# Kernel optimization log

Measured on AMD Instinct MI355X. Metric: run time of the kernel, lower is better.

The kernel has to match this reference:

```python
import jax, jax.numpy as jnp
import numpy as np

N_NODES = 50000
N_EDGES = 600000
N_GRAPHS = 2000
IN_FEATS = 64
HIDDEN = 128


def setup_inputs() -> dict:
    key = jax.random.key(0)
    ks = jax.random.split(key, 16)
    d = {}
    d["feats_node"] = jax.random.normal(ks[0], (N_NODES, IN_FEATS), jnp.float32)
    d["feats_graph"] = jax.random.normal(ks[1], (N_GRAPHS, 3), jnp.float32)
    s = 0.05
    d["W1"] = jax.random.normal(ks[2], (IN_FEATS, HIDDEN), jnp.float32) * s
    d["b1"] = jnp.zeros((HIDDEN,), jnp.float32)
    d["W2"] = jax.random.normal(ks[3], (HIDDEN, HIDDEN), jnp.float32) * s
    d["b2"] = jnp.zeros((HIDDEN,), jnp.float32)
    d["W3"] = jax.random.normal(ks[4], (HIDDEN, HIDDEN), jnp.float32) * s
    d["b3"] = jnp.zeros((HIDDEN,), jnp.float32)
    d["Wl1"] = jax.random.normal(ks[5], (HIDDEN + 3, 2 * HIDDEN), jnp.float32) * s
    d["bl1"] = jnp.zeros((2 * HIDDEN,), jnp.float32)
    d["Wl2"] = jax.random.normal(ks[6], (2 * HIDDEN, 2 * HIDDEN), jnp.float32) * s
    d["bl2"] = jnp.zeros((2 * HIDDEN,), jnp.float32)
    d["Wl3"] = jax.random.normal(ks[7], (2 * HIDDEN, 1), jnp.float32) * s
    d["bl3"] = jnp.zeros((1,), jnp.float32)
    d["src"] = jax.random.randint(ks[8], (N_EDGES,), 0, N_NODES, jnp.int32)
    d["dst"] = jax.random.randint(ks[9], (N_EDGES,), 0, N_NODES, jnp.int32)
    d["graph_ids"] = jnp.sort(jax.random.randint(ks[10], (N_NODES,), 0, N_GRAPHS, jnp.int32))
    return d


def reference(feats_node, feats_graph, W1, b1, W2, b2, W3, b3,
              Wl1, bl1, Wl2, bl2, Wl3, bl3, src, dst, graph_ids):
    N = feats_node.shape[0]
    ones_e = jnp.ones((src.shape[0],), feats_node.dtype)
    # DGL GraphConv norm='both': symmetric degree normalization, degrees clamped to >=1
    deg_out = jax.ops.segment_sum(ones_e, src, num_segments=N)
    deg_in = jax.ops.segment_sum(ones_e, dst, num_segments=N)
    c_out = jax.lax.rsqrt(jnp.maximum(deg_out, 1.0))[:, None]  # [N,1]
    c_in = jax.lax.rsqrt(jnp.maximum(deg_in, 1.0))[:, None]

    def gconv(x, W, b):
        h = x * c_out                                   # scale by src out-degree
        agg = jax.ops.segment_sum(h[src], dst, num_segments=N)  # gather + scatter-add
        return (agg * c_in) @ W + b

    x = jax.nn.relu(gconv(feats_node, W1, b1))
    x = jax.nn.relu(gconv(x, W2, b2))
    y_nodes = gconv(x, W3, b3)                          # [N, HIDDEN]

    # readout_nodes op='mean' over batched graphs
    G = feats_graph.shape[0]
    sum_y = jax.ops.segment_sum(y_nodes, graph_ids, num_segments=G)
    cnt = jax.ops.segment_sum(jnp.ones((N,), y_nodes.dtype), graph_ids, num_segments=G)
    mean_y = sum_y / jnp.maximum(cnt, 1.0)[:, None]     # [G, HIDDEN]

    y = jnp.concatenate([mean_y, feats_graph], axis=1)  # [G, HIDDEN+3]
    y = jax.nn.relu(y @ Wl1 + bl1)
    y = jax.nn.relu(y @ Wl2 + bl2)
    return (y @ Wl3 + bl3).reshape(-1)                  # [G]
```

## Files before the change

### kernel.cpp

```cpp
#include <hip/hip_runtime.h>

constexpr int NNODES = 50000;
constexpr int NEDGES = 600000;
constexpr int NGRAPH = 2000;
constexpr int F0     = 64;
constexpr int H      = 128;
constexpr int H2     = 256;
constexpr int NB     = 49;

static __device__ __forceinline__ void fma4(float4& acc, float s, const float4& w) {
    acc.x = fmaf(s, w.x, acc.x);
    acc.y = fmaf(s, w.y, acc.y);
    acc.z = fmaf(s, w.z, acc.z);
    acc.w = fmaf(s, w.w, acc.w);
}

__global__ void k_deg(const int* __restrict__ src, const int* __restrict__ dst,
                      int* __restrict__ dout, int* __restrict__ din) {
    int t = blockIdx.x * 256 + threadIdx.x;
    if (t * 4 >= NEDGES) return;
    int4 s4 = ((const int4*)src)[t];
    int4 d4 = ((const int4*)dst)[t];
    atomicAdd(&dout[s4.x], 1);
    atomicAdd(&dout[s4.y], 1);
    atomicAdd(&dout[s4.z], 1);
    atomicAdd(&dout[s4.w], 1);
    atomicAdd(&din[d4.x], 1);
    atomicAdd(&din[d4.y], 1);
    atomicAdd(&din[d4.z], 1);
    atomicAdd(&din[d4.w], 1);
}

__global__ __launch_bounds__(1024) void k_scan1(const int* __restrict__ deg,
                                                int* __restrict__ row_start,
                                                int* __restrict__ partials,
                                                float* __restrict__ c_in) {
    __shared__ int wsum[16];
    int idx  = blockIdx.x * 1024 + threadIdx.x;
    int lane = threadIdx.x & 63;
    int wid  = threadIdx.x >> 6;
    int v = (idx < NNODES) ? deg[idx] : 0;
    if (idx < NNODES) c_in[idx] = rsqrtf(fmaxf((float)v, 1.0f));
    int incl = v;
#pragma unroll
    for (int off = 1; off < 64; off <<= 1) {
        int t = __shfl_up(incl, off);
        if (lane >= off) incl += t;
    }
    if (lane == 63) wsum[wid] = incl;
    __syncthreads();
    if (wid == 0) {
        int w = (lane < 16) ? wsum[lane] : 0;
        int wincl = w;
#pragma unroll
        for (int off = 1; off < 16; off <<= 1) {
            int t = __shfl_up(wincl, off);
            if (lane >= off) wincl += t;
        }
        if (lane < 16) wsum[lane] = wincl - w;
    }
    __syncthreads();
    int excl = wsum[wid] + incl - v;
    if (idx < NNODES) row_start[idx] = excl;
    if (threadIdx.x == 1023) partials[blockIdx.x] = excl + v;
}

__global__ void k_scan2(int* __restrict__ partials) {
    int lane = threadIdx.x;
    int v = (lane < NB) ? partials[lane] : 0;
    int incl = v;
#pragma unroll
    for (int off = 1; off < 64; off <<= 1) {
        int t = __shfl_up(incl, off);
        if (lane >= off) incl += t;
    }
    if (lane < NB) partials[lane] = incl - v;
    if (lane == NB - 1) partials[NB] = incl;
}

__global__ __launch_bounds__(1024) void k_scan3(int* __restrict__ row_start,
                                                const int* __restrict__ partials,
                                                const int* __restrict__ dout,
                                                float* __restrict__ c_out) {
    int idx = blockIdx.x * 1024 + threadIdx.x;
    if (idx < NNODES) {
        row_start[idx] += partials[blockIdx.x];
        c_out[idx] = rsqrtf(fmaxf((float)dout[idx], 1.0f));
    } else if (idx == NNODES) {
        row_start[NNODES] = partials[NB];
    }
}

__global__ void k_fill(const int* __restrict__ src, const int* __restrict__ dst,
                       const int* __restrict__ row_start, int* __restrict__ cursor,
                       int* __restrict__ csr_src) {
    int t = blockIdx.x * 256 + threadIdx.x;
    if (t * 4 >= NEDGES) return;
    int4 s4 = ((const int4*)src)[t];
    int4 d4 = ((const int4*)dst)[t];
    int p;
    p = atomicAdd(&cursor[d4.x], 1); csr_src[row_start[d4.x] + p] = s4.x;
    p = atomicAdd(&cursor[d4.y], 1); csr_src[row_start[d4.y] + p] = s4.y;
    p = atomicAdd(&cursor[d4.z], 1); csr_src[row_start[d4.z] + p] = s4.z;
    p = atomicAdd(&cursor[d4.w], 1); csr_src[row_start[d4.w] + p] = s4.w;
}

__global__ void k_gbounds(const int* __restrict__ gids, int* __restrict__ gstart) {
    int n = blockIdx.x * 256 + threadIdx.x;
    if (n > NNODES) return;
    if (n == 0) {
        int g0 = gids[0];
        for (int g = 0; g <= g0; ++g) gstart[g] = 0;
    } else if (n == NNODES) {
        int gl = gids[NNODES - 1];
        for (int g = gl + 1; g <= NGRAPH; ++g) gstart[g] = NNODES;
    } else {
        int a = gids[n - 1], b = gids[n];
        for (int g = a + 1; g <= b; ++g) gstart[g] = n;
    }
}

template <int F>
__global__ __launch_bounds__(256) void k_gather(const float* __restrict__ x,
                                                const float* __restrict__ c_out,
                                                const int* __restrict__ row_start,
                                                const int* __restrict__ csr_src,
                                                float* __restrict__ agg) {
    int wid  = (blockIdx.x * 256 + threadIdx.x) >> 6;
    int lane = threadIdx.x & 63;
    int h = lane >> 5, q = lane & 31;
    if (wid >= NNODES) return;
    int beg = row_start[wid], end = row_start[wid + 1];
    if (F == 128) {
        const float4* x4 = (const float4*)x;
        float4 acc = make_float4(0.f, 0.f, 0.f, 0.f);
        for (int i = beg + h; i < end; i += 2) {
            int s = csr_src[i];
            float co = c_out[s];
            float4 v = x4[(long)s * 32 + q];
            acc.x += v.x * co;
            acc.y += v.y * co;
            acc.z += v.z * co;
            acc.w += v.w * co;
        }
        acc.x += __shfl_xor(acc.x, 32);
        acc.y += __shfl_xor(acc.y, 32);
        acc.z += __shfl_xor(acc.z, 32);
        acc.w += __shfl_xor(acc.w, 32);
        if (h == 0) ((float4*)agg)[(long)wid * 32 + q] = acc;
    } else {
        const float2* x2 = (const float2*)x;
        float2 acc = make_float2(0.f, 0.f);
        for (int i = beg + h; i < end; i += 2) {
            int s = csr_src[i];
            float co = c_out[s];
            float2 v = x2[(long)s * 32 + q];
            acc.x += v.x * co;
            acc.y += v.y * co;
        }
        acc.x += __shfl_xor(acc.x, 32);
        acc.y += __shfl_xor(acc.y, 32);
        if (h == 0) ((float2*)agg)[(long)wid * 32 + q] = acc;
    }
}

template <int K, bool RELU>
__global__ __launch_bounds__(512) void k_gemm(const float* __restrict__ A,
                                              const float* __restrict__ c_in,
                                              const float* __restrict__ W,
                                              const float* __restrict__ b,
                                              float* __restrict__ out) {
    __shared__ float sW[K * H];
    for (int i = threadIdx.x; i < K * (H / 4); i += 512)
        ((float4*)sW)[i] = ((const float4*)W)[i];
    __syncthreads();

    const int c = threadIdx.x & 31;
    const int r = threadIdx.x >> 5;
    const long base = (long)blockIdx.x * 128 + r * 8;

    float4 acc[8];
#pragma unroll
    for (int i = 0; i < 8; ++i) acc[i] = make_float4(0.f, 0.f, 0.f, 0.f);

    const float4* Ap = (const float4*)A + base * (K / 4);

    for (int k4 = 0; k4 < K / 4; ++k4) {
        const float4 w0 = *(const float4*)&sW[(4 * k4 + 0) * H + 4 * c];
        const float4 w1 = *(const float4*)&sW[(4 * k4 + 1) * H + 4 * c];
        const float4 w2 = *(const float4*)&sW[(4 * k4 + 2) * H + 4 * c];
        const float4 w3 = *(const float4*)&sW[(4 * k4 + 3) * H + 4 * c];
#pragma unroll
        for (int i = 0; i < 8; ++i) {
            float4 a = Ap[(long)i * (K / 4) + k4];
            fma4(acc[i], a.x, w0);
            fma4(acc[i], a.y, w1);
            fma4(acc[i], a.z, w2);
            fma4(acc[i], a.w, w3);
        }
    }

    const float4 bv = ((const float4*)b)[c];
#pragma unroll
    for (int i = 0; i < 8; ++i) {
        long n = base + i;
        if (n < NNODES) {
            float ci = c_in[n];
            float4 res;
            res.x = fmaf(acc[i].x, ci, bv.x);
            res.y = fmaf(acc[i].y, ci, bv.y);
            res.z = fmaf(acc[i].z, ci, bv.z);
            res.w = fmaf(acc[i].w, ci, bv.w);
            if (RELU) {
                res.x = fmaxf(res.x, 0.f);
                res.y = fmaxf(res.y, 0.f);
                res.z = fmaxf(res.z, 0.f);
                res.w = fmaxf(res.w, 0.f);
            }
            ((float4*)out)[n * (H / 4) + c] = res;
        }
    }
}

__global__ void k_readout(const float* __restrict__ y, const int* __restrict__ gstart,
                          float* __restrict__ mean) {
    int g = blockIdx.x * 2 + (threadIdx.x >> 7);
    int j = threadIdx.x & 127;
    if (g >= NGRAPH) return;
    int beg = gstart[g], end = gstart[g + 1];
    float acc = 0.f;
    for (int n = beg; n < end; ++n) acc += y[(long)n * H + j];
    mean[g * H + j] = acc / fmaxf((float)(end - beg), 1.0f);
}

__global__ void k_mlp1(const float* __restrict__ mean, const float* __restrict__ fg,
                       const float* __restrict__ Wl1, const float* __restrict__ bl1,
                       float* __restrict__ h1) {
    int g  = blockIdx.x * 4 + (threadIdx.x >> 6);
    int jq = threadIdx.x & 63;
    if (g >= NGRAPH) return;
    float4 acc = ((const float4*)bl1)[jq];
    for (int k = 0; k < H; ++k)
        fma4(acc, mean[g * H + k], ((const float4*)(Wl1 + (long)k * H2))[jq]);
    for (int k = 0; k < 3; ++k)
        fma4(acc, fg[g * 3 + k], ((const float4*)(Wl1 + (long)(H + k) * H2))[jq]);
    acc.x = fmaxf(acc.x, 0.f); acc.y = fmaxf(acc.y, 0.f);
    acc.z = fmaxf(acc.z, 0.f); acc.w = fmaxf(acc.w, 0.f);
    ((float4*)h1)[g * 64 + jq] = acc;
}

__global__ void k_mlp2(const float* __restrict__ h1, const float* __restrict__ Wl2,
                       const float* __restrict__ bl2, float* __restrict__ h2) {
    int g  = blockIdx.x * 4 + (threadIdx.x >> 6);
    int jq = threadIdx.x & 63;
    if (g >= NGRAPH) return;
    float4 acc = ((const float4*)bl2)[jq];
    for (int k = 0; k < H2; ++k)
        fma4(acc, h1[g * H2 + k], ((const float4*)(Wl2 + (long)k * H2))[jq]);
    acc.x = fmaxf(acc.x, 0.f); acc.y = fmaxf(acc.y, 0.f);
    acc.z = fmaxf(acc.z, 0.f); acc.w = fmaxf(acc.w, 0.f);
    ((float4*)h2)[g * 64 + jq] = acc;
}

__global__ void k_mlp3(const float* __restrict__ h2, const float* __restrict__ Wl3,
                       const float* __restrict__ bl3, float* __restrict__ out) {
    int gw = (blockIdx.x * 256 + threadIdx.x) >> 6;
    int lane = threadIdx.x & 63;
    if (gw >= NGRAPH) return;
    float sum = 0.0f;
    for (int k = lane; k < H2; k += 64)
        sum += h2[gw * H2 + k] * Wl3[k];
    for (int off = 32; off; off >>= 1)
        sum += __shfl_down(sum, off);
    if (lane == 0) out[gw] = sum + bl3[0];
}

extern "C" void kernel_launch(void* const* d_in, const int* in_sizes, int n_in,
                              void* d_out, int out_size, void* d_ws, size_t ws_size,
                              hipStream_t stream) {
    const float* feats_node  = (const float*)d_in[0];
    const float* feats_graph = (const float*)d_in[1];
    const float* W1 = (const float*)d_in[2];
    const float* b1 = (const float*)d_in[3];
    const float* W2 = (const float*)d_in[4];
    const float* b2 = (const float*)d_in[5];
    const float* W3 = (const float*)d_in[6];
    const float* b3 = (const float*)d_in[7];
    const float* Wl1 = (const float*)d_in[8];
    const float* bl1 = (const float*)d_in[9];
    const float* Wl2 = (const float*)d_in[10];
    const float* bl2 = (const float*)d_in[11];
    const float* Wl3 = (const float*)d_in[12];
    const float* bl3 = (const float*)d_in[13];
    const int* src  = (const int*)d_in[14];
    const int* dst  = (const int*)d_in[15];
    const int* gids = (const int*)d_in[16];
    float* out = (float*)d_out;

    float* ws = (float*)d_ws;
    float* c_out     = ws;
    float* c_in      = c_out + 50048;
    float* A         = c_in + 50048;
    float* B         = A + (size_t)NNODES * H;
    int*   row_start = (int*)(B + (size_t)NNODES * H);
    int*   csr_src   = row_start + 50176;
    int*   cursor    = csr_src + NEDGES;
    int*   gstart    = cursor + 50176;
    int*   partials  = gstart + 2048;
    int*   dout      = partials + 64;
    int*   din       = dout + 50048;
    float* mean      = (float*)(din + 50048);
    float* h1        = mean + (size_t)NGRAPH * H;
    float* h2        = h1 + (size_t)NGRAPH * H2;

    hipMemsetAsync(dout, 0, 2 * 50048 * sizeof(int), stream);
    k_deg<<<(NEDGES / 4 + 255) / 256, 256, 0, stream>>>(src, dst, dout, din);

    k_scan1<<<NB, 1024, 0, stream>>>(din, row_start, partials, c_in);
    k_scan2<<<1, 64, 0, stream>>>(partials);
    k_scan3<<<NB, 1024, 0, stream>>>(row_start, partials, dout, c_out);
    hipMemsetAsync(cursor, 0, 50176 * sizeof(int), stream);
    k_fill<<<(NEDGES / 4 + 255) / 256, 256, 0, stream>>>(src, dst, row_start, cursor, csr_src);
    k_gbounds<<<(NNODES + 256) / 256, 256, 0, stream>>>(gids, gstart);

    const int GEMM_GRID = (NNODES + 127) / 128;

    k_gather<F0><<<NNODES / 4, 256, 0, stream>>>(feats_node, c_out, row_start, csr_src, A);
    k_gemm<F0, true><<<GEMM_GRID, 512, 0, stream>>>(A, c_in, W1, b1, B);

    k_gather<H><<<NNODES / 4, 256, 0, stream>>>(B, c_out, row_start, csr_src, A);
    k_gemm<H, true><<<GEMM_GRID, 512, 0, stream>>>(A, c_in, W2, b2, B);

    k_gather<H><<<NNODES / 4, 256, 0, stream>>>(B, c_out, row_start, csr_src, A);
    k_gemm<H, false><<<GEMM_GRID, 512, 0, stream>>>(A, c_in, W3, b3, B);

    k_readout<<<NGRAPH / 2, 256, 0, stream>>>(B, gstart, mean);

    k_mlp1<<<NGRAPH / 4, 256, 0, stream>>>(mean, feats_graph, Wl1, bl1, h1);
    k_mlp2<<<NGRAPH / 4, 256, 0, stream>>>(h1, Wl2, bl2, h2);
    k_mlp3<<<(NGRAPH * 64 + 255) / 256, 256, 0, stream>>>(h2, Wl3, bl3, out);
}
```

Before: 458.9 us.

## Fuse readout and MLP head, fold cursor reset, remap gather lanes

Measured after the change: 428.6 us. 1.07x faster.

```diff
diff --git a/kernel.cpp b/kernel.cpp
--- a/kernel.cpp
+++ b/kernel.cpp
@@ -81,11 +81,13 @@
 __global__ __launch_bounds__(1024) void k_scan3(int* __restrict__ row_start,
                                                 const int* __restrict__ partials,
                                                 const int* __restrict__ dout,
-                                                float* __restrict__ c_out) {
+                                                float* __restrict__ c_out,
+                                                int* __restrict__ cursor) {
     int idx = blockIdx.x * 1024 + threadIdx.x;
     if (idx < NNODES) {
         row_start[idx] += partials[blockIdx.x];
         c_out[idx] = rsqrtf(fmaxf((float)dout[idx], 1.0f));
+        cursor[idx] = 0;
     } else if (idx == NNODES) {
         row_start[NNODES] = partials[NB];
     }
@@ -121,55 +123,66 @@
 }
 
 template <int F>
-__global__ __launch_bounds__(256) void k_gather(const float* __restrict__ x,
-                                                const float* __restrict__ c_out,
-                                                const int* __restrict__ row_start,
-                                                const int* __restrict__ csr_src,
-                                                float* __restrict__ agg) {
+static __device__ __forceinline__ void gather_body(const float* __restrict__ x,
+                                                   const float* __restrict__ c_out,
+                                                   const int* __restrict__ row_start,
+                                                   const int* __restrict__ csr_src,
+                                                   float* __restrict__ agg) {
     int wid  = (blockIdx.x * 256 + threadIdx.x) >> 6;
     int lane = threadIdx.x & 63;
-    int h = lane >> 5, q = lane & 31;
     if (wid >= NNODES) return;
     int beg = row_start[wid], end = row_start[wid + 1];
     if (F == 128) {
-        const float4* x4 = (const float4*)x;
-        float4 acc = make_float4(0.f, 0.f, 0.f, 0.f);
-        for (int i = beg + h; i < end; i += 2) {
+        const float2* x2 = (const float2*)x;
+        float2 acc = make_float2(0.f, 0.f);
+#pragma unroll 4
+        for (int i = beg; i < end; ++i) {
             int s = csr_src[i];
             float co = c_out[s];
-            float4 v = x4[(long)s * 32 + q];
+            float2 v = x2[(long)s * 64 + lane];
             acc.x += v.x * co;
             acc.y += v.y * co;
-            acc.z += v.z * co;
-            acc.w += v.w * co;
-        }
-        acc.x += __shfl_xor(acc.x, 32);
-        acc.y += __shfl_xor(acc.y, 32);
-        acc.z += __shfl_xor(acc.z, 32);
-        acc.w += __shfl_xor(acc.w, 32);
-        if (h == 0) ((float4*)agg)[(long)wid * 32 + q] = acc;
+        }
+        ((float2*)agg)[(long)wid * 64 + lane] = acc;
     } else {
-        const float2* x2 = (const float2*)x;
-        float2 acc = make_float2(0.f, 0.f);
-        for (int i = beg + h; i < end; i += 2) {
+        float acc = 0.f;
+#pragma unroll 4
+        for (int i = beg; i < end; ++i) {
             int s = csr_src[i];
-            float co = c_out[s];
-            float2 v = x2[(long)s * 32 + q];
-            acc.x += v.x * co;
-            acc.y += v.y * co;
-        }
-        acc.x += __shfl_xor(acc.x, 32);
-        acc.y += __shfl_xor(acc.y, 32);
-        if (h == 0) ((float2*)agg)[(long)wid * 32 + q] = acc;
-    }
+            acc += x[(long)s * F + lane] * c_out[s];
+        }
+        agg[(long)wid * F + lane] = acc;
+    }
+}
+
+__global__ __launch_bounds__(256) void k_gather1(const float* __restrict__ x,
+                                                 const float* __restrict__ c_out,
+                                                 const int* __restrict__ row_start,
+                                                 const int* __restrict__ csr_src,
+                                                 float* __restrict__ agg) {
+    gather_body<F0>(x, c_out, row_start, csr_src, agg);
+}
+__global__ __launch_bounds__(256) void k_gather2(const float* __restrict__ x,
+                                                 const float* __restrict__ c_out,
+                                                 const int* __restrict__ row_start,
+                                                 const int* __restrict__ csr_src,
+                                                 float* __restrict__ agg) {
+    gather_body<H>(x, c_out, row_start, csr_src, agg);
+}
+__global__ __launch_bounds__(256) void k_gather3(const float* __restrict__ x,
+                                                 const float* __restrict__ c_out,
+                                                 const int* __restrict__ row_start,
+                                                 const int* __restrict__ csr_src,
+                                                 float* __restrict__ agg) {
+    gather_body<H>(x, c_out, row_start, csr_src, agg);
 }
 
 template <int K, bool RELU>
-__global__ __launch_bounds__(512) void k_gemm(const float* __restrict__ A,
-                                              const float* __restrict__ c_in,
-                                              const float* __restrict__ W,
-                                              const float* __restrict__ b,
-                                              float* __restrict__ out) {
+static __device__ __forceinline__ void gemm_body(const float* __restrict__ A,
+                                                 const float* __restrict__ c_in,
+                                                 const float* __restrict__ W,
+                                                 const float* __restrict__ b,
+                                                 float* __restrict__ out) {
     __shared__ float sW[K * H];
     for (int i = threadIdx.x; i < K * (H / 4); i += 512)
         ((float4*)sW)[i] = ((const float4*)W)[i];
@@ -222,57 +235,89 @@
     }
 }
 
-__global__ void k_readout(const float* __restrict__ y, const int* __restrict__ gstart,
-                          float* __restrict__ mean) {
-    int g = blockIdx.x * 2 + (threadIdx.x >> 7);
-    int j = threadIdx.x & 127;
-    if (g >= NGRAPH) return;
-    int beg = gstart[g], end = gstart[g + 1];
-    float acc = 0.f;
-    for (int n = beg; n < end; ++n) acc += y[(long)n * H + j];
-    mean[g * H + j] = acc / fmaxf((float)(end - beg), 1.0f);
-}
-
-__global__ void k_mlp1(const float* __restrict__ mean, const float* __restrict__ fg,
-                       const float* __restrict__ Wl1, const float* __restrict__ bl1,
-                       float* __restrict__ h1) {
-    int g  = blockIdx.x * 4 + (threadIdx.x >> 6);
-    int jq = threadIdx.x & 63;
-    if (g >= NGRAPH) return;
-    float4 acc = ((const float4*)bl1)[jq];
-    for (int k = 0; k < H; ++k)
-        fma4(acc, mean[g * H + k], ((const float4*)(Wl1 + (long)k * H2))[jq]);
-    for (int k = 0; k < 3; ++k)
-        fma4(acc, fg[g * 3 + k], ((const float4*)(Wl1 + (long)(H + k) * H2))[jq]);
-    acc.x = fmaxf(acc.x, 0.f); acc.y = fmaxf(acc.y, 0.f);
-    acc.z = fmaxf(acc.z, 0.f); acc.w = fmaxf(acc.w, 0.f);
-    ((float4*)h1)[g * 64 + jq] = acc;
-}
-
-__global__ void k_mlp2(const float* __restrict__ h1, const float* __restrict__ Wl2,
-                       const float* __restrict__ bl2, float* __restrict__ h2) {
-    int g  = blockIdx.x * 4 + (threadIdx.x >> 6);
-    int jq = threadIdx.x & 63;
-    if (g >= NGRAPH) return;
-    float4 acc = ((const float4*)bl2)[jq];
-    for (int k = 0; k < H2; ++k)
-        fma4(acc, h1[g * H2 + k], ((const float4*)(Wl2 + (long)k * H2))[jq]);
-    acc.x = fmaxf(acc.x, 0.f); acc.y = fmaxf(acc.y, 0.f);
-    acc.z = fmaxf(acc.z, 0.f); acc.w = fmaxf(acc.w, 0.f);
-    ((float4*)h2)[g * 64 + jq] = acc;
-}
-
-__global__ void k_mlp3(const float* __restrict__ h2, const float* __restrict__ Wl3,
-                       const float* __restrict__ bl3, float* __restrict__ out) {
-    int gw = (blockIdx.x * 256 + threadIdx.x) >> 6;
-    int lane = threadIdx.x & 63;
-    if (gw >= NGRAPH) return;
-    float sum = 0.0f;
-    for (int k = lane; k < H2; k += 64)
-        sum += h2[gw * H2 + k] * Wl3[k];
-    for (int off = 32; off; off >>= 1)
-        sum += __shfl_down(sum, off);
-    if (lane == 0) out[gw] = sum + bl3[0];
+__global__ __launch_bounds__(512) void k_gemm1(const float* __restrict__ A,
+                                               const float* __restrict__ c_in,
+                                               const float* __restrict__ W,
+                                               const float* __restrict__ b,
+                                               float* __restrict__ out) {
+    gemm_body<F0, true>(A, c_in, W, b, out);
+}
+__global__ __launch_bounds__(512) void k_gemm2(const float* __restrict__ A,
+                                               const float* __restrict__ c_in,
+                                               const float* __restrict__ W,
+                                               const float* __restrict__ b,
+                                               float* __restrict__ out) {
+    gemm_body<H, true>(A, c_in, W, b, out);
+}
+__global__ __launch_bounds__(512) void k_gemm3(const float* __restrict__ A,
+                                               const float* __restrict__ c_in,
+                                               const float* __restrict__ W,
+                                               const float* __restrict__ b,
+                                               float* __restrict__ out) {
+    gemm_body<H, false>(A, c_in, W, b, out);
+}
+
+__global__ __launch_bounds__(256) void k_head(const float* __restrict__ y,
+                                              const int* __restrict__ gstart,
+                                              const float* __restrict__ fg,
+                                              const float* __restrict__ Wl1,
+                                              const float* __restrict__ bl1,
+                                              const float* __restrict__ Wl2,
+                                              const float* __restrict__ bl2,
+                                              const float* __restrict__ Wl3,
+                                              const float* __restrict__ bl3,
+                                              float* __restrict__ out) {
+    __shared__ float smean[4][H];
+    __shared__ float sh1[4][H2];
+    __shared__ float sh2[4][H2];
+
+    const int w    = threadIdx.x >> 6;
+    const int lane = threadIdx.x & 63;
+    const int g    = blockIdx.x * 4 + w;
+
+    {
+        int beg = gstart[g], end = gstart[g + 1];
+        const float2* y2 = (const float2*)y;
+        float2 acc = make_float2(0.f, 0.f);
+        for (int n = beg; n < end; ++n) {
+            float2 v = y2[(long)n * 64 + lane];
+            acc.x += v.x;
+            acc.y += v.y;
+        }
+        float inv = 1.0f / fmaxf((float)(end - beg), 1.0f);
+        ((float2*)smean[w])[lane] = make_float2(acc.x * inv, acc.y * inv);
+    }
+
+    {
+        float4 acc = ((const float4*)bl1)[lane];
+        for (int k = 0; k < H; ++k)
+            fma4(acc, smean[w][k], ((const float4*)(Wl1 + (long)k * H2))[lane]);
+#pragma unroll
+        for (int k = 0; k < 3; ++k)
+            fma4(acc, fg[g * 3 + k], ((const float4*)(Wl1 + (long)(H + k) * H2))[lane]);
+        acc.x = fmaxf(acc.x, 0.f); acc.y = fmaxf(acc.y, 0.f);
+        acc.z = fmaxf(acc.z, 0.f); acc.w = fmaxf(acc.w, 0.f);
+        ((float4*)sh1[w])[lane] = acc;
+    }
+
+    {
+        float4 acc = ((const float4*)bl2)[lane];
+        for (int k = 0; k < H2; ++k)
+            fma4(acc, sh1[w][k], ((const float4*)(Wl2 + (long)k * H2))[lane]);
+        acc.x = fmaxf(acc.x, 0.f); acc.y = fmaxf(acc.y, 0.f);
+        acc.z = fmaxf(acc.z, 0.f); acc.w = fmaxf(acc.w, 0.f);
+        ((float4*)sh2[w])[lane] = acc;
+    }
+
+    {
+        float sum = sh2[w][lane] * Wl3[lane]
+                  + sh2[w][lane + 64] * Wl3[lane + 64]
+                  + sh2[w][lane + 128] * Wl3[lane + 128]
+                  + sh2[w][lane + 192] * Wl3[lane + 192];
+        for (int off = 32; off; off >>= 1)
+            sum += __shfl_down(sum, off);
+        if (lane == 0) out[g] = sum + bl3[0];
+    }
 }
 
 extern "C" void kernel_launch(void* const* d_in, const int* in_sizes, int n_in,
@@ -309,34 +354,27 @@
     int*   partials  = gstart + 2048;
     int*   dout      = partials + 64;
     int*   din       = dout + 50048;
-    float* mean      = (float*)(din + 50048);
-    float* h1        = mean + (size_t)NGRAPH * H;
-    float* h2        = h1 + (size_t)NGRAPH * H2;
 
     hipMemsetAsync(dout, 0, 2 * 50048 * sizeof(int), stream);
     k_deg<<<(NEDGES / 4 + 255) / 256, 256, 0, stream>>>(src, dst, dout, din);
 
     k_scan1<<<NB, 1024, 0, stream>>>(din, row_start, partials, c_in);
     k_scan2<<<1, 64, 0, stream>>>(partials);
-    k_scan3<<<NB, 1024, 0, stream>>>(row_start, partials, dout, c_out);
-    hipMemsetAsync(cursor, 0, 50176 * sizeof(int), stream);
+    k_scan3<<<NB, 1024, 0, stream>>>(row_start, partials, dout, c_out, cursor);
     k_fill<<<(NEDGES / 4 + 255) / 256, 256, 0, stream>>>(src, dst, row_start, cursor, csr_src);
     k_gbounds<<<(NNODES + 256) / 256, 256, 0, stream>>>(gids, gstart);
 
     const int GEMM_GRID = (NNODES + 127) / 128;
 
-    k_gather<F0><<<NNODES / 4, 256, 0, stream>>>(feats_node, c_out, row_start, csr_src, A);
-    k_gemm<F0, true><<<GEMM_GRID, 512, 0, stream>>>(A, c_in, W1, b1, B);
-
-    k_gather<H><<<NNODES / 4, 256, 0, stream>>>(B, c_out, row_start, csr_src, A);
-    k_gemm<H, true><<<GEMM_GRID, 512, 0, stream>>>(A, c_in, W2, b2, B);
-
-    k_gather<H><<<NNODES / 4, 256, 0, stream>>>(B, c_out, row_start, csr_src, A);
-    k_gemm<H, false><<<GEMM_GRID, 512, 0, stream>>>(A, c_in, W3, b3, B);
-
-    k_readout<<<NGRAPH / 2, 256, 0, stream>>>(B, gstart, mean);
-
-    k_mlp1<<<NGRAPH / 4, 256, 0, stream>>>(mean, feats_graph, Wl1, bl1, h1);
-    k_mlp2<<<NGRAPH / 4, 256, 0, stream>>>(h1, Wl2, bl2, h2);
-    k_mlp3<<<(NGRAPH * 64 + 255) / 256, 256, 0, stream>>>(h2, Wl3, bl3, out);
-}
+    k_gather1<<<NNODES / 4, 256, 0, stream>>>(feats_node, c_out, row_start, csr_src, A);
+    k_gemm1<<<GEMM_GRID, 512, 0, stream>>>(A, c_in, W1, b1, B);
+
+    k_gather2<<<NNODES / 4, 256, 0, stream>>>(B, c_out, row_start, csr_src, A);
+    k_gemm2<<<GEMM_GRID, 512, 0, stream>>>(A, c_in, W2, b2, B);
+
+    k_gather3<<<NNODES / 4, 256, 0, stream>>>(B, c_out, row_start, csr_src, A);
+    k_gemm3<<<GEMM_GRID, 512, 0, stream>>>(A, c_in, W3, b3, B);
+
+    k_head<<<NGRAPH / 4, 256, 0, stream>>>(B, gstart, feats_graph,
+                                           Wl1, bl1, Wl2, bl2, Wl3, bl3, out);
+}
```
